# Optimization experiments

Measured on AMD Instinct MI355X. Metric: run time of the kernel, lower is better.

## Reference

```python
import jax, jax.numpy as jnp
import numpy as np

N, E, D, DH, MH, MO = 100000, 1600000, 128, 512, 512, 128
EPS_BN = 1e-5
EPS_LN = 1e-5


def setup_inputs() -> dict:
    key = jax.random.key(0)
    ks = jax.random.split(key, 16)
    def lin(k, fan_in, shape):
        return jax.random.normal(k, shape, jnp.float32) / np.sqrt(fan_in)
    return {
        'x': jax.random.normal(ks[0], (N, D), jnp.float32),
        'src': jax.random.randint(ks[1], (E,), 0, N, jnp.int32),
        'dst': jax.random.randint(ks[2], (E,), 0, N, jnp.int32),
        'gcn_w': lin(ks[3], D, (D, D)),
        'gcn_b': jnp.zeros((D,), jnp.float32),
        'ff_w1': lin(ks[4], D, (D, DH)),
        'ff_b1': jnp.zeros((DH,), jnp.float32),
        'ln_g': jnp.ones((DH,), jnp.float32),
        'ln_b': jnp.zeros((DH,), jnp.float32),
        'ff_w2': lin(ks[5], DH, (DH, D)),
        'ff_b2': jnp.zeros((D,), jnp.float32),
        'fc1_w': lin(ks[6], D, (D, MH)),
        'fc1_b': jnp.zeros((MH,), jnp.float32),
        'bn1_g': jnp.ones((MH,), jnp.float32),
        'bn1_b': jnp.zeros((MH,), jnp.float32),
        'fc2_w': lin(ks[7], MH, (MH, MH)),
        'fc2_b': jnp.zeros((MH,), jnp.float32),
        'bn2_g': jnp.ones((MH,), jnp.float32),
        'bn2_b': jnp.zeros((MH,), jnp.float32),
        'fc3_w': lin(ks[8], MH, (MH, MO)),
        'fc3_b': jnp.zeros((MO,), jnp.float32),
        'bn3_g': jnp.ones((MO,), jnp.float32),
        'bn3_b': jnp.zeros((MO,), jnp.float32),
        'fc4_w': lin(ks[9], MO, (MO, 1)),
        'fc4_b': jnp.zeros((1,), jnp.float32),
    }


def _gelu(x):
    return jax.nn.gelu(x, approximate=False)  # torch nn.GELU default (erf)


def _batchnorm(x, g, b):
    # BatchNorm1d in training mode: batch statistics, biased variance
    m = jnp.mean(x, axis=0)
    v = jnp.var(x, axis=0)
    return (x - m) * jax.lax.rsqrt(v + EPS_BN) * g + b


def reference(x, src, dst, gcn_w, gcn_b, ff_w1, ff_b1, ln_g, ln_b, ff_w2, ff_b2,
              fc1_w, fc1_b, bn1_g, bn1_b, fc2_w, fc2_b, bn2_g, bn2_b,
              fc3_w, fc3_b, bn3_g, bn3_b, fc4_w, fc4_b):
    n = x.shape[0]
    ones = jnp.ones(src.shape[0], x.dtype)
    out_deg = jnp.clip(jax.ops.segment_sum(ones, src, num_segments=n), 1.0)
    in_deg = jnp.clip(jax.ops.segment_sum(ones, dst, num_segments=n), 1.0)
    # GraphConv, norm='both': left-normalize, aggregate, matmul (in==out), right-normalize, bias
    h = x * (out_deg ** -0.5)[:, None]
    agg = jax.ops.segment_sum(h[src], dst, num_segments=n)  # [N, D]
    h = agg @ gcn_w
    h = h * (in_deg ** -0.5)[:, None] + gcn_b
    # FeedForwardLayer: lin1 -> GELU -> LayerNorm -> lin2
    f = _gelu(h @ ff_w1 + ff_b1)
    mu = jnp.mean(f, axis=-1, keepdims=True)
    var = jnp.var(f, axis=-1, keepdims=True)
    f = (f - mu) * jax.lax.rsqrt(var + EPS_LN) * ln_g + ln_b
    h = f @ ff_w2 + ff_b2  # [N, D]
    # MLP head
    h = _batchnorm(_gelu(h @ fc1_w + fc1_b), bn1_g, bn1_b)
    h = _batchnorm(_gelu(h @ fc2_w + fc2_b), bn2_g, bn2_b)
    h = _batchnorm(_gelu(h @ fc3_w + fc3_b), bn3_g, bn3_b)
    return h @ fc4_w + fc4_b  # [N, 1]
```

## Files before the change

kernel.cpp:

```cpp
#include <hip/hip_runtime.h>
#include <hip/hip_bf16.h>

#define N_NODES 100000
#define NPAD    100096
#define NRB     782
#define E_EDGES 1600000
#define NBLK_SCAN 98

#define HNR  4
#define HP   64
#define HCHK 25000
#define HRSZ 32768

#define AS1 __attribute__((address_space(1)))
#define AS3 __attribute__((address_space(3)))

typedef unsigned int   uint;
typedef unsigned short ushort;
typedef __attribute__((ext_vector_type(8))) short bfx8;
typedef __attribute__((ext_vector_type(4))) float fx4;

__device__ __forceinline__ float bf2f(ushort u) {
    return __uint_as_float(((uint)u) << 16);
}
__device__ __forceinline__ ushort f2bf(float f) {
    uint x = __float_as_uint(f);
    return (ushort)((x + 0x7FFFu + ((x >> 16) & 1u)) >> 16);
}
__device__ __forceinline__ float gelu_fast(float x) {
    float u = 1.5957691f * __builtin_fmaf(0.044715f * x * x, x, x);
    return x / (1.0f + __expf(-u));
}
__device__ __forceinline__ float wave_sum(float v) {
    #pragma unroll
    for (int m = 1; m < 64; m <<= 1) v += __shfl_xor(v, m, 64);
    return v;
}
__device__ __forceinline__ int xcd_swz(int orig, int nwg) {
    int q = nwg >> 3, r = nwg & 7;
    int x = orig & 7, o = orig >> 3;
    return (x < r ? x * (q + 1) : r * (q + 1) + (x - r) * q) + o;
}

__global__ void k_hist(const int* __restrict__ idx, uint* __restrict__ part)
{
    __shared__ uint h[HRSZ / 2];
    int c = blockIdx.x & (HP - 1);
    int r = blockIdx.x / HP;
    int t = threadIdx.x;
    for (int i = t; i < HRSZ / 2; i += 256) h[i] = 0u;
    __syncthreads();
    int base = r << 15;
    int e0 = c * HCHK;
    for (int e = e0 + t; e < e0 + HCHK; e += 256) {
        int v = idx[e] - base;
        if ((uint)v < (uint)HRSZ)
            atomicAdd(&h[v >> 1], 1u << ((v & 1) * 16));
    }
    __syncthreads();
    uint* dst = part + ((size_t)blockIdx.x << 14);
    for (int i = t; i < HRSZ / 2; i += 256) dst[i] = h[i];
}

__global__ void k_degmerge(const uint* __restrict__ partO, const uint* __restrict__ partI,
                           int* __restrict__ inc, float* __restrict__ oscale,
                           float* __restrict__ ininv)
{
    int n = blockIdx.x * 256 + threadIdx.x;
    if (n >= NPAD) return;
    int r = n >> 15, i = (n & 32767) >> 1, hi = (n & 1) * 16;
    const uint* po = partO + ((size_t)(r * HP) << 14) + i;
    const uint* pi = partI + ((size_t)(r * HP) << 14) + i;
    uint so = 0, si = 0;
    for (int c = 0; c < HP; ++c) {
        so += (po[(size_t)c << 14] >> hi) & 0xffffu;
        si += (pi[(size_t)c << 14] >> hi) & 0xffffu;
    }
    inc[n] = (int)si;
    oscale[n] = rsqrtf((float)max((int)so, 1));
    ininv[n] = rsqrtf((float)max((int)si, 1));
}

__global__ void k_scan1(const int* __restrict__ inc, int* __restrict__ coff, int* __restrict__ btot)
{
    __shared__ int a[1024], bsh[1024];
    int t = threadIdx.x;
    int i = blockIdx.x * 1024 + t;
    a[t] = (i < N_NODES) ? inc[i] : 0;
    __syncthreads();
    int* s = a; int* d = bsh;
    for (int dd = 1; dd < 1024; dd <<= 1) {
        int v = s[t] + ((t >= dd) ? s[t - dd] : 0);
        d[t] = v;
        __syncthreads();
        int* tmp = s; s = d; d = tmp;
    }
    if (i < N_NODES) coff[i + 1] = s[t];
    if (t == 1023) btot[blockIdx.x] = s[t];
}

__global__ void k_scan2(int* __restrict__ btot)
{
    __shared__ int a[128], bsh[128];
    int t = threadIdx.x;
    a[t] = (t < NBLK_SCAN) ? btot[t] : 0;
    __syncthreads();
    int* s = a; int* d = bsh;
    for (int dd = 1; dd < 128; dd <<= 1) {
        int v = s[t] + ((t >= dd) ? s[t - dd] : 0);
        d[t] = v;
        __syncthreads();
        int* tmp = s; s = d; d = tmp;
    }
    if (t < NBLK_SCAN) btot[t] = s[t];
}

__global__ void k_scan3(int* __restrict__ coff, const int* __restrict__ btot)
{
    int i = blockIdx.x * 256 + threadIdx.x;
    if (i == 0) coff[0] = 0;
    if (i < N_NODES) {
        int blk = i >> 10;
        if (blk > 0) coff[i + 1] += btot[blk - 1];
    }
}

__global__ void k_fill(const int* __restrict__ src, const int* __restrict__ dst,
                       const int* __restrict__ coff, int* __restrict__ cur, int* __restrict__ eidx)
{
    int e = blockIdx.x * 256 + threadIdx.x;
    if (e < E_EDGES) {
        int d = dst[e];
        int p = coff[d] + atomicAdd(&cur[d], 1);
        eidx[p] = src[e];
    }
}

__global__ void k_xhat(const float* __restrict__ x, const float* __restrict__ oscale,
                       ushort* __restrict__ xh)
{
    size_t i = (size_t)blockIdx.x * 256 + threadIdx.x;
    size_t e0 = i * 4;
    int row = (int)(e0 >> 7);
    uint2 o;
    if (row < N_NODES) {
        float4 v = *(const float4*)(x + e0);
        float s = oscale[row];
        o.x = (uint)f2bf(v.x * s) | ((uint)f2bf(v.y * s) << 16);
        o.y = (uint)f2bf(v.z * s) | ((uint)f2bf(v.w * s) << 16);
    } else {
        o.x = 0u; o.y = 0u;
    }
    *(uint2*)(xh + e0) = o;
}

__global__ void k_agg(const int* __restrict__ off, const int* __restrict__ eidx,
                      const ushort* __restrict__ xh, ushort* __restrict__ agg)
{
    int wid = threadIdx.x >> 6, lane = threadIdx.x & 63;
    int r = blockIdx.x * 4 + wid;
    if (r >= NPAD) return;
    int f = lane & 15;
    int g = lane >> 4;
    float a[8] = {0.f, 0.f, 0.f, 0.f, 0.f, 0.f, 0.f, 0.f};
    if (r < N_NODES) {
        int s = off[r], e = off[r + 1];
        for (int i = s + g; i < e; i += 4) {
            int sv = eidx[i];
            bfx8 v = *(const bfx8*)(xh + (size_t)sv * 128 + f * 8);
            #pragma unroll
            for (int k = 0; k < 8; ++k) a[k] += bf2f((ushort)v[k]);
        }
    }
    #pragma unroll
    for (int k = 0; k < 8; ++k) {
        a[k] += __shfl_xor(a[k], 16, 64);
        a[k] += __shfl_xor(a[k], 32, 64);
    }
    if (g == 0) {
        bfx8 o;
        #pragma unroll
        for (int k = 0; k < 8; ++k) o[k] = (short)f2bf(a[k]);
        *(bfx8*)(agg + (size_t)r * 128 + f * 8) = o;
    }
}

__global__ void k_wT(const float* __restrict__ W, int K, int M, ushort* __restrict__ Wt)
{
    int id = blockIdx.x * 256 + threadIdx.x;
    if (id < K * M) {
        int m = id / K, k = id - m * K;
        Wt[id] = f2bf(W[(size_t)k * M + m]);
    }
}

__global__ void k_wT_ln(const float* __restrict__ W, const float* __restrict__ g,
                        const float* __restrict__ b, const float* __restrict__ b2,
                        ushort* __restrict__ Wt, float* __restrict__ u, float* __restrict__ t)
{
    int wid = threadIdx.x >> 6, lane = threadIdx.x & 63;
    int m = blockIdx.x * 4 + wid;
    if (m >= 128) return;
    float us = 0.f, ts = 0.f;
    for (int k = lane; k < 512; k += 64) {
        float w = W[(size_t)k * 128 + m];
        float gk = g[k], bk = b[k];
        Wt[(size_t)m * 512 + k] = f2bf(gk * w);
        us += gk * w; ts += bk * w;
    }
    us = wave_sum(us); ts = wave_sum(ts);
    if (lane == 0) { u[m] = us; t[m] = ts + b2[m]; }
}

template <int K1, int EPI1, int STATS2>
__global__ __launch_bounds__(256, 2) void k_fused(
    const ushort* __restrict__ A1, const ushort* __restrict__ B1t,
    const ushort* __restrict__ B2t, ushort* __restrict__ C,
    const float* __restrict__ c1v0, const float* __restrict__ r1v0,
    const float* __restrict__ r1v1, const float* __restrict__ c1v1,
    const float* __restrict__ bias2,
    float* __restrict__ lnS, float* __restrict__ lnC,
    float* __restrict__ pS, float* __restrict__ pQ)
{
    __shared__ __align__(16) char smem[32768 + 32768 + 2048];
    char* A2 = smem;
    char* S  = smem + 32768;
    float* st_s = (float*)(smem + 65536);
    float* st_q = (float*)(smem + 65536 + 1024);

    const int rb = xcd_swz(blockIdx.x, gridDim.x);
    const int tid = threadIdx.x;
    const int lane = tid & 63;
    const int wid = tid >> 6;
    const int m0 = (wid >> 1) * 64;
    const int n0 = (wid & 1) * 64;
    const int frl = lane & 15;
    const int kg = lane >> 4;

    char* As = S;
    char* Bs = S + 16384;
    fx4 acc[4][4] = {};
    const ushort* Arow0 = A1 + (size_t)(rb * 128) * K1;

    for (int kb = 0; kb < K1; kb += 64) {
        #pragma unroll
        for (int c = 0; c < 4; ++c) {
            int b = c * 4096 + tid * 16;
            int row = b >> 7;
            int cibs = (b & 127) ^ ((row & 7) << 4);
            const char* ga = (const char*)(Arow0 + (size_t)row * K1 + kb) + cibs;
            const char* gb = (const char*)(B1t + (size_t)row * K1 + kb) + cibs;
            char* la = As + c * 4096 + (wid << 10);
            char* lb = Bs + c * 4096 + (wid << 10);
            __builtin_amdgcn_global_load_lds((const AS1 void*)ga, (AS3 void*)la, 16, 0, 0);
            __builtin_amdgcn_global_load_lds((const AS1 void*)gb, (AS3 void*)lb, 16, 0, 0);
        }
        __syncthreads();
        #pragma unroll
        for (int kk = 0; kk < 2; ++kk) {
            bfx8 av[4], bv[4];
            #pragma unroll
            for (int i = 0; i < 4; ++i) {
                int ar = m0 + i * 16 + frl;
                int ab = (ar * 128 + kk * 64 + kg * 16) ^ ((ar & 7) << 4);
                av[i] = *(const bfx8*)(As + ab);
                int br = n0 + i * 16 + frl;
                int bb = (br * 128 + kk * 64 + kg * 16) ^ ((br & 7) << 4);
                bv[i] = *(const bfx8*)(Bs + bb);
            }
            #pragma unroll
            for (int i = 0; i < 4; ++i)
                #pragma unroll
                for (int j = 0; j < 4; ++j)
                    acc[i][j] = __builtin_amdgcn_mfma_f32_16x16x32_bf16(av[i], bv[j], acc[i][j], 0, 0, 0);
        }
        __syncthreads();
    }

    #pragma unroll
    for (int j = 0; j < 4; ++j) {
        int colL = n0 + j * 16 + frl;
        float c0 = c1v0[colL];
        float c1 = (EPI1 == 3) ? c1v1[colL] : 0.f;
        #pragma unroll
        for (int i = 0; i < 4; ++i) {
            int rbaseL = m0 + i * 16 + kg * 4;
            #pragma unroll
            for (int r = 0; r < 4; ++r) {
                float v = acc[i][j][r];
                int rowL = rbaseL + r;
                int grow = rb * 128 + rowL;
                if (EPI1 == 0) v = v * r1v0[grow] + c0;
                else           v = r1v0[grow] * v + r1v1[grow] * c1 + c0;
                *(ushort*)(A2 + rowL * 256 + ((colL * 2) ^ ((rowL & 7) << 4))) = f2bf(v);
            }
        }
    }
    __syncthreads();

    float rs = 0.f, rq = 0.f;
    const int rowR = tid >> 1, halfR = tid & 1;

    for (int cb2 = 0; cb2 < 4; ++cb2) {
        #pragma unroll
        for (int c = 0; c < 8; ++c) {
            int b = c * 4096 + tid * 16;
            int row = b >> 8;
            int cibs = (b & 255) ^ ((row & 7) << 4);
            const char* gb = (const char*)(B2t + (size_t)(cb2 * 128 + row) * 128) + cibs;
            char* lb = S + c * 4096 + (wid << 10);
            __builtin_amdgcn_global_load_lds((const AS1 void*)gb, (AS3 void*)lb, 16, 0, 0);
        }
        __syncthreads();

        fx4 a2[4][4] = {};
        #pragma unroll
        for (int kk = 0; kk < 4; ++kk) {
            bfx8 av[4], bv[4];
            int c2 = kk * 64 + kg * 16;
            #pragma unroll
            for (int i = 0; i < 4; ++i) {
                int ar = m0 + i * 16 + frl;
                av[i] = *(const bfx8*)(A2 + ar * 256 + (c2 ^ ((ar & 7) << 4)));
                int br = n0 + i * 16 + frl;
                bv[i] = *(const bfx8*)(S + br * 256 + (c2 ^ ((br & 7) << 4)));
            }
            #pragma unroll
            for (int i = 0; i < 4; ++i)
                #pragma unroll
                for (int j = 0; j < 4; ++j)
                    a2[i][j] = __builtin_amdgcn_mfma_f32_16x16x32_bf16(av[i], bv[j], a2[i][j], 0, 0, 0);
        }
        __syncthreads();

        float sL[4] = {0.f, 0.f, 0.f, 0.f}, qL[4] = {0.f, 0.f, 0.f, 0.f};
        #pragma unroll
        for (int j = 0; j < 4; ++j) {
            int colL = n0 + j * 16 + frl;
            float bcol = bias2[cb2 * 128 + colL];
            #pragma unroll
            for (int i = 0; i < 4; ++i) {
                int rbaseL = m0 + i * 16 + kg * 4;
                #pragma unroll
                for (int r = 0; r < 4; ++r) {
                    float v = gelu_fast(a2[i][j][r] + bcol);
                    int rowL = rbaseL + r;
                    if (STATS2 == 1) {
                        if (rb * 128 + rowL < N_NODES) { sL[j] += v; qL[j] += v * v; }
                    }
                    *(ushort*)(S + rowL * 256 + ((colL * 2) ^ ((rowL & 7) << 4))) = f2bf(v);
                }
            }
            if (STATS2 == 1) {
                float s = sL[j], q = qL[j];
                s += __shfl_xor(s, 16, 64); s += __shfl_xor(s, 32, 64);
                q += __shfl_xor(q, 16, 64); q += __shfl_xor(q, 32, 64);
                if (kg == 0) {
                    st_s[(wid >> 1) * 128 + n0 + j * 16 + frl] = s;
                    st_q[(wid >> 1) * 128 + n0 + j * 16 + frl] = q;
                }
            }
        }
        __syncthreads();

        {
            int r2 = tid >> 4;
            int s2 = tid & 15;
            #pragma unroll
            for (int pass = 0; pass < 8; ++pass) {
                int rowL = pass * 16 + r2;
                int boff = rowL * 256 + ((s2 * 16) ^ ((rowL & 7) << 4));
                bfx8 v = *(const bfx8*)(S + boff);
                *(bfx8*)((char*)(C + (size_t)(rb * 128 + rowL) * 512 + cb2 * 128) + s2 * 16) = v;
            }
        }
        if (STATS2 == 1 && tid < 128) {
            size_t pidx = ((size_t)rb * 4 + cb2) * 128 + tid;
            pS[pidx] = st_s[tid] + st_s[128 + tid];
            pQ[pidx] = st_q[tid] + st_q[128 + tid];
        }
        if (STATS2 == 2) {
            #pragma unroll
            for (int ss = 0; ss < 8; ++ss) {
                int boff = rowR * 256 + (((halfR * 64 + ss * 8) * 2) ^ ((rowR & 7) << 4));
                bfx8 v = *(const bfx8*)(S + boff);
                #pragma unroll
                for (int k2 = 0; k2 < 8; ++k2) {
                    float f = bf2f((ushort)v[k2]);
                    rs += f; rq += f * f;
                }
            }
        }
        __syncthreads();
    }

    if (STATS2 == 2) {
        rs += __shfl_xor(rs, 1, 64);
        rq += __shfl_xor(rq, 1, 64);
        if (halfR == 0) {
            float mean = rs * (1.f / 512.f);
            float var = fmaxf(rq * (1.f / 512.f) - mean * mean, 0.f);
            float sr = rsqrtf(var + 1e-5f);
            int grow = rb * 128 + rowR;
            lnS[grow] = sr;
            lnC[grow] = -mean * sr;
        }
    }
}

template <int EPI, int STATS>
__global__ __launch_bounds__(256, 4) void k_gemm(
    const ushort* __restrict__ A, const ushort* __restrict__ Bt,
    ushort* __restrict__ C, int K, int M,
    const float* __restrict__ colv0, const float* __restrict__ rowv0,
    float* __restrict__ pS, float* __restrict__ pQ, int grb0)
{
    __shared__ __align__(16) char smem[32768 + (STATS == 1 ? 1024 : 0)];
    char* AsB = smem;
    char* BsB = smem + 16384;

    const int nwg = gridDim.x;
    const int wgid = xcd_swz(blockIdx.x, nwg);
    const int nCB = M >> 7;
    const int cb = wgid % nCB;
    const int rb = wgid / nCB;
    const int tid = threadIdx.x;
    const int lane = tid & 63;
    const int wid = tid >> 6;
    const int m0 = (wid >> 1) * 64;
    const int n0 = (wid & 1) * 64;
    const int frl = lane & 15;
    const int kg = lane >> 4;

    float* statsf = (float*)(smem + 32768);
    if (STATS == 1 && tid < 128) { statsf[tid] = 0.f; statsf[128 + tid] = 0.f; }

    fx4 acc[4][4] = {};

    const ushort* Arow0 = A + (size_t)(rb * 128) * K;
    const ushort* Brow0 = Bt + (size_t)(cb * 128) * K;

    for (int kb = 0; kb < K; kb += 64) {
        #pragma unroll
        for (int c = 0; c < 4; ++c) {
            int b = c * 4096 + tid * 16;
            int row = b >> 7;
            int cibs = (b & 127) ^ ((row & 7) << 4);
            const char* ga = (const char*)(Arow0 + (size_t)row * K + kb) + cibs;
            const char* gb = (const char*)(Brow0 + (size_t)row * K + kb) + cibs;
            char* la = AsB + c * 4096 + (wid << 10);
            char* lb = BsB + c * 4096 + (wid << 10);
            __builtin_amdgcn_global_load_lds((const AS1 void*)ga, (AS3 void*)la, 16, 0, 0);
            __builtin_amdgcn_global_load_lds((const AS1 void*)gb, (AS3 void*)lb, 16, 0, 0);
        }
        __syncthreads();
        #pragma unroll
        for (int kk = 0; kk < 2; ++kk) {
            bfx8 av[4], bv[4];
            #pragma unroll
            for (int i = 0; i < 4; ++i) {
                int ar = m0 + i * 16 + frl;
                int ab = (ar * 128 + kk * 64 + kg * 16) ^ ((ar & 7) << 4);
                av[i] = *(const bfx8*)(AsB + ab);
                int br = n0 + i * 16 + frl;
                int bb = (br * 128 + kk * 64 + kg * 16) ^ ((br & 7) << 4);
                bv[i] = *(const bfx8*)(BsB + bb);
            }
            #pragma unroll
            for (int i = 0; i < 4; ++i)
                #pragma unroll
                for (int j = 0; j < 4; ++j)
                    acc[i][j] = __builtin_amdgcn_mfma_f32_16x16x32_bf16(av[i], bv[j], acc[i][j], 0, 0, 0);
        }
        __syncthreads();
    }

    float sL[4] = {0.f, 0.f, 0.f, 0.f}, qL[4] = {0.f, 0.f, 0.f, 0.f};
    #pragma unroll
    for (int j = 0; j < 4; ++j) {
        int colL = n0 + j * 16 + frl;
        float c0 = colv0[cb * 128 + colL];
        #pragma unroll
        for (int i = 0; i < 4; ++i) {
            int rbaseL = m0 + i * 16 + kg * 4;
            #pragma unroll
            for (int r = 0; r < 4; ++r) {
                float v = acc[i][j][r];
                int rowL = rbaseL + r;
                int grow = (grb0 + rb) * 128 + rowL;
                if (EPI == 0) v = v * rowv0[grow] + c0;
                else          v = gelu_fast(v + c0);
                if (STATS == 1) {
                    if (grow < N_NODES) { sL[j] += v; qL[j] += v * v; }
                }
                int boff = rowL * 256 + ((colL * 2) ^ ((rowL & 7) << 4));
                *(ushort*)(smem + boff) = f2bf(v);
            }
        }
    }
    if (STATS == 1) {
        #pragma unroll
        for (int j = 0; j < 4; ++j) {
            float s = sL[j], q = qL[j];
            s += __shfl_xor(s, 16, 64); s += __shfl_xor(s, 32, 64);
            q += __shfl_xor(q, 16, 64); q += __shfl_xor(q, 32, 64);
            if (kg == 0) {
                atomicAdd(&statsf[n0 + j * 16 + frl], s);
                atomicAdd(&statsf[128 + n0 + j * 16 + frl], q);
            }
        }
    }
    __syncthreads();
    {
        int r2 = tid >> 4;
        int s2 = tid & 15;
        #pragma unroll
        for (int pass = 0; pass < 8; ++pass) {
            int rowL = pass * 16 + r2;
            int boff = rowL * 256 + ((s2 * 16) ^ ((rowL & 7) << 4));
            bfx8 v = *(const bfx8*)(smem + boff);
            *(bfx8*)((char*)(C + (size_t)(rb * 128 + rowL) * M + cb * 128) + s2 * 16) = v;
        }
    }
    if (STATS == 1 && tid < 128) {
        size_t pidx = ((size_t)(grb0 + rb) * nCB + cb) * 128 + tid;
        pS[pidx] = statsf[tid];
        pQ[pidx] = statsf[128 + tid];
    }
}

__global__ void k_colmerge(const float* __restrict__ pS, const float* __restrict__ pQ,
                           float* __restrict__ oS, float* __restrict__ oQ, int M)
{
    int wid = threadIdx.x >> 6, lane = threadIdx.x & 63;
    int m = blockIdx.x * 4 + wid;
    if (m >= M) return;
    int nCB = M >> 7, cb = m >> 7, colL = m & 127;
    float s = 0.f, q = 0.f;
    for (int rb = lane; rb < NRB; rb += 64) {
        size_t idx = ((size_t)rb * nCB + cb) * 128 + colL;
        s += pS[idx]; q += pQ[idx];
    }
    s = wave_sum(s); q = wave_sum(q);
    if (lane == 0) { oS[m] = s; oQ[m] = q; }
}

__global__ void k_fold(const float* __restrict__ W, const float* __restrict__ bw,
                       const float* __restrict__ g, const float* __restrict__ bb,
                       const float* __restrict__ sum, const float* __restrict__ sqs,
                       int K, int M, ushort* __restrict__ WtO, float* __restrict__ bO)
{
    int wid = threadIdx.x >> 6, lane = threadIdx.x & 63;
    int m = blockIdx.x * 4 + wid;
    if (m >= M) return;
    float acc = 0.f;
    for (int k = lane; k < K; k += 64) {
        float mean = sum[k] * (1.f / (float)N_NODES);
        float var = sqs[k] * (1.f / (float)N_NODES) - mean * mean;
        float s = g[k] * rsqrtf(var + 1e-5f);
        float t = bb[k] - mean * s;
        float w = W[(size_t)k * M + m];
        WtO[(size_t)m * K + k] = f2bf(w * s);
        acc += t * w;
    }
    acc = wave_sum(acc);
    if (lane == 0) bO[m] = bw[m] + acc;
}

__global__ void k_out(const ushort* __restrict__ m3, const ushort* __restrict__ w4,
                      const float* __restrict__ b4, float* __restrict__ out)
{
    int wid = threadIdx.x >> 6, lane = threadIdx.x & 63;
    int r = blockIdx.x * 4 + wid;
    if (r >= N_NODES) return;
    uint u = *(const uint*)(m3 + (size_t)r * 128 + lane * 2);
    uint w = *(const uint*)(w4 + lane * 2);
    float acc = bf2f((ushort)(u & 0xffffu)) * bf2f((ushort)(w & 0xffffu))
              + bf2f((ushort)(u >> 16)) * bf2f((ushort)(w >> 16));
    acc = wave_sum(acc);
    if (lane == 0) out[r] = acc + b4[0];
}

extern "C" void kernel_launch(void* const* d_in, const int* in_sizes, int n_in,
                              void* d_out, int out_size, void* d_ws, size_t ws_size,
                              hipStream_t stream)
{
    const float* x     = (const float*)d_in[0];
    const int*   src   = (const int*)d_in[1];
    const int*   dst   = (const int*)d_in[2];
    const float* gcn_w = (const float*)d_in[3];
    const float* gcn_b = (const float*)d_in[4];
    const float* ff_w1 = (const float*)d_in[5];
    const float* ff_b1 = (const float*)d_in[6];
    const float* ln_g  = (const float*)d_in[7];
    const float* ln_b  = (const float*)d_in[8];
    const float* ff_w2 = (const float*)d_in[9];
    const float* ff_b2 = (const float*)d_in[10];
    const float* fc1_w = (const float*)d_in[11];
    const float* fc1_b = (const float*)d_in[12];
    const float* bn1_g = (const float*)d_in[13];
    const float* bn1_b = (const float*)d_in[14];
    const float* fc2_w = (const float*)d_in[15];
    const float* fc2_b = (const float*)d_in[16];
    const float* bn2_g = (const float*)d_in[17];
    const float* bn2_b = (const float*)d_in[18];
    const float* fc3_w = (const float*)d_in[19];
    const float* fc3_b = (const float*)d_in[20];
    const float* bn3_g = (const float*)d_in[21];
    const float* bn3_b = (const float*)d_in[22];
    const float* fc4_w = (const float*)d_in[23];
    const float* fc4_b = (const float*)d_in[24];
    float* out = (float*)d_out;
    (void)in_sizes; (void)n_in; (void)out_size;

    char* base = (char*)d_ws;
    char* p = base;
    auto alloc = [&](size_t bytes) -> char* {
        char* r = p;
        p += (bytes + 255) & ~(size_t)255;
        return r;
    };
    int*    inc    = (int*)alloc((size_t)NPAD * 4);
    int*    cur    = (int*)alloc((size_t)NPAD * 4);
    int*    coff   = (int*)alloc(((size_t)NPAD + 1) * 4);
    int*    btot   = (int*)alloc(128 * 4);
    int*    eidx   = (int*)alloc((size_t)E_EDGES * 4);
    float*  oscale = (float*)alloc((size_t)NPAD * 4);
    float*  ininv  = (float*)alloc((size_t)NPAD * 4);
    float*  bns    = (float*)alloc(6 * 512 * 4);
    float*  b2p    = (float*)alloc(512 * 4);
    float*  b3p    = (float*)alloc(128 * 4);
    float*  b4p    = (float*)alloc(4);
    float*  lnS    = (float*)alloc((size_t)NPAD * 4);
    float*  lnC    = (float*)alloc((size_t)NPAD * 4);
    float*  lnU    = (float*)alloc(128 * 4);
    float*  lnT    = (float*)alloc(128 * 4);
    float*  pS     = (float*)alloc((size_t)4 * NPAD * 4);
    float*  pQ     = (float*)alloc((size_t)4 * NPAD * 4);
    ushort* gwT    = (ushort*)alloc(128 * 128 * 2);
    ushort* ff1T   = (ushort*)alloc(512 * 128 * 2);
    ushort* ff2T   = (ushort*)alloc(128 * 512 * 2);
    ushort* fc1T   = (ushort*)alloc(512 * 128 * 2);
    ushort* fc2T   = (ushort*)alloc(512 * 512 * 2);
    ushort* fc3T   = (ushort*)alloc(128 * 512 * 2);
    ushort* w4t    = (ushort*)alloc(128 * 2);
    ushort* buf1   = (ushort*)alloc((size_t)NPAD * 128 * 2);
    ushort* bufC   = (ushort*)alloc((size_t)NPAD * 512 * 2);

    size_t used = (size_t)(p - base);
    bool   sep  = (used + (size_t)NPAD * 512 * 2) <= ws_size;
    ushort* m2  = sep ? (ushort*)alloc((size_t)NPAD * 512 * 2) : bufC;

    uint* partO = (uint*)bufC;
    uint* partI = partO + (size_t)HNR * HP * (HRSZ / 2);
    ushort* xh  = bufC;
    ushort* agg = buf1;

    float* bn1s = bns;
    float* bn1q = bns + 512;
    float* bn2s = bns + 1024;
    float* bn2q = bns + 1536;
    float* bn3s = bns + 2048;
    float* bn3q = bns + 2560;

    hipMemsetAsync(cur, 0, (size_t)NPAD * 4, stream);

    k_hist<<<HNR * HP, 256, 0, stream>>>(src, partO);
    k_hist<<<HNR * HP, 256, 0, stream>>>(dst, partI);
    k_degmerge<<<(NPAD + 255) / 256, 256, 0, stream>>>(partO, partI, inc, oscale, ininv);
    k_scan1<<<NBLK_SCAN, 1024, 0, stream>>>(inc, coff, btot);
    k_scan2<<<1, 128, 0, stream>>>(btot);
    k_scan3<<<(N_NODES + 255) / 256, 256, 0, stream>>>(coff, btot);
    k_fill<<<E_EDGES / 256, 256, 0, stream>>>(src, dst, coff, cur, eidx);
    k_xhat<<<(NPAD / 256) * 32, 256, 0, stream>>>(x, oscale, xh);
    k_agg<<<NPAD / 4, 256, 0, stream>>>(coff, eidx, xh, agg);

    k_wT<<<(128 * 128) / 256, 256, 0, stream>>>(gcn_w, 128, 128, gwT);
    k_wT<<<(128 * 512) / 256, 256, 0, stream>>>(ff_w1, 128, 512, ff1T);
    k_wT<<<(128 * 512) / 256, 256, 0, stream>>>(fc1_w, 128, 512, fc1T);
    k_wT_ln<<<32, 256, 0, stream>>>(ff_w2, ln_g, ln_b, ff_b2, ff2T, lnU, lnT);

    k_fused<128, 0, 2><<<NRB, 256, 0, stream>>>(agg, gwT, ff1T, bufC,
                                                gcn_b, ininv, nullptr, nullptr, ff_b1,
                                                lnS, lnC, nullptr, nullptr);
    k_fused<512, 3, 1><<<NRB, 256, 0, stream>>>(bufC, ff2T, fc1T, bufC,
                                                lnT, lnS, lnC, lnU, fc1_b,
                                                nullptr, nullptr, pS, pQ);
    k_colmerge<<<128, 256, 0, stream>>>(pS, pQ, bn1s, bn1q, 512);
    k_fold<<<512 / 4, 256, 0, stream>>>(fc2_w, fc2_b, bn1_g, bn1_b, bn1s, bn1q, 512, 512, fc2T, b2p);
    if (sep) {
        k_gemm<1, 1><<<4 * NRB, 256, 0, stream>>>(bufC, fc2T, m2, 512, 512,
                                                  b2p, nullptr, pS, pQ, 0);
    } else {
        const int cOff[6] = {0, 195, 390, 585, 780, 782};
        for (int c = 0; c < 5; ++c) {
            int rb0 = cOff[c], nrb = cOff[c + 1] - rb0;
            k_gemm<1, 1><<<nrb * 4, 256, 0, stream>>>(bufC + (size_t)rb0 * 128 * 512, fc2T,
                                                      buf1, 512, 512,
                                                      b2p, nullptr, pS, pQ, rb0);
            hipMemcpyAsync(bufC + (size_t)rb0 * 128 * 512, buf1,
                           (size_t)nrb * 128 * 512 * 2, hipMemcpyDeviceToDevice, stream);
        }
    }
    k_colmerge<<<128, 256, 0, stream>>>(pS, pQ, bn2s, bn2q, 512);
    k_fold<<<128 / 4, 256, 0, stream>>>(fc3_w, fc3_b, bn2_g, bn2_b, bn2s, bn2q, 512, 128, fc3T, b3p);
    k_gemm<1, 1><<<NRB, 256, 0, stream>>>(m2, fc3T, buf1, 512, 128,
                                          b3p, nullptr, pS, pQ, 0);
    k_colmerge<<<32, 256, 0, stream>>>(pS, pQ, bn3s, bn3q, 128);
    k_fold<<<1, 256, 0, stream>>>(fc4_w, fc4_b, bn3_g, bn3_b, bn3s, bn3q, 128, 1, w4t, b4p);
    k_out<<<N_NODES / 4, 256, 0, stream>>>(buf1, w4t, b4p, out);
}
```

Baseline: 679.1 us.

## Replace global-atomic CSR fill with two-pass bucketed partition and local-atomic scatter

```diff
diff --git a/kernel.cpp b/kernel.cpp
--- a/kernel.cpp
+++ b/kernel.cpp
@@ -11,6 +11,9 @@
 #define HP   64
 #define HCHK 25000
 #define HRSZ 32768
+
+#define NBK  196
+#define PCHK 6250
 
 #define AS1 __attribute__((address_space(1)))
 #define AS3 __attribute__((address_space(3)))
@@ -125,14 +128,73 @@
     }
 }
 
-__global__ void k_fill(const int* __restrict__ src, const int* __restrict__ dst,
-                       const int* __restrict__ coff, int* __restrict__ cur, int* __restrict__ eidx)
-{
-    int e = blockIdx.x * 256 + threadIdx.x;
-    if (e < E_EDGES) {
-        int d = dst[e];
-        int p = coff[d] + atomicAdd(&cur[d], 1);
-        eidx[p] = src[e];
+__global__ void k_curinit(const int* __restrict__ coff, int* __restrict__ gcur)
+{
+    int t = threadIdx.x;
+    if (t < NBK) gcur[t] = coff[t << 9];
+}
+
+__global__ __launch_bounds__(256) void k_part(const int* __restrict__ src, const int* __restrict__ dst,
+                                              int* __restrict__ gcur, uint* __restrict__ tmp)
+{
+    __shared__ int cnt[NBK], rcnt[NBK], base[NBK], loff[NBK];
+    __shared__ int sa[256], sb[256];
+    __shared__ uint arr[PCHK];
+    int t = threadIdx.x;
+    if (t < NBK) { cnt[t] = 0; rcnt[t] = 0; }
+    __syncthreads();
+    int e0 = blockIdx.x * PCHK;
+    for (int e = e0 + t; e < e0 + PCHK; e += 256)
+        atomicAdd(&cnt[dst[e] >> 9], 1);
+    __syncthreads();
+    sa[t] = (t < NBK) ? cnt[t] : 0;
+    __syncthreads();
+    int* s = sa; int* d = sb;
+    for (int dd = 1; dd < 256; dd <<= 1) {
+        int v = s[t] + ((t >= dd) ? s[t - dd] : 0);
+        d[t] = v;
+        __syncthreads();
+        int* w = s; s = d; d = w;
+    }
+    if (t < NBK) {
+        loff[t] = s[t] - cnt[t];
+        base[t] = atomicAdd(&gcur[t], cnt[t]);
+    }
+    __syncthreads();
+    for (int e = e0 + t; e < e0 + PCHK; e += 256) {
+        int dv = dst[e];
+        int b = dv >> 9;
+        int r = atomicAdd(&rcnt[b], 1);
+        arr[loff[b] + r] = ((uint)src[e] << 9) | (uint)(dv & 511);
+    }
+    __syncthreads();
+    for (int b = 0; b < NBK; ++b) {
+        int n = cnt[b], lo = loff[b], gb = base[b];
+        for (int i = t; i < n; i += 256)
+            tmp[gb + i] = arr[lo + i];
+    }
+}
+
+__global__ __launch_bounds__(256) void k_fill2(const uint* __restrict__ tmp, const int* __restrict__ coff,
+                                               int* __restrict__ eidx)
+{
+    __shared__ int lco[512];
+    __shared__ int lcnt[512];
+    int b = blockIdx.x, t = threadIdx.x;
+    int n0 = b << 9;
+    for (int i = t; i < 512; i += 256) {
+        int node = n0 + i;
+        lco[i] = (node <= N_NODES) ? coff[node] : E_EDGES;
+        lcnt[i] = 0;
+    }
+    __syncthreads();
+    int s0 = coff[n0];
+    int s1 = (n0 + 512 <= N_NODES) ? coff[n0 + 512] : E_EDGES;
+    for (int e = s0 + t; e < s1; e += 256) {
+        uint v = tmp[e];
+        int dl = v & 511;
+        int r = atomicAdd(&lcnt[dl], 1);
+        eidx[lco[dl] + r] = (int)(v >> 9);
     }
 }
 
@@ -621,9 +683,9 @@
         return r;
     };
     int*    inc    = (int*)alloc((size_t)NPAD * 4);
-    int*    cur    = (int*)alloc((size_t)NPAD * 4);
     int*    coff   = (int*)alloc(((size_t)NPAD + 1) * 4);
     int*    btot   = (int*)alloc(128 * 4);
+    int*    gcur   = (int*)alloc(256 * 4);
     int*    eidx   = (int*)alloc((size_t)E_EDGES * 4);
     float*  oscale = (float*)alloc((size_t)NPAD * 4);
     float*  ininv  = (float*)alloc((size_t)NPAD * 4);
@@ -653,6 +715,7 @@
 
     uint* partO = (uint*)bufC;
     uint* partI = partO + (size_t)HNR * HP * (HRSZ / 2);
+    uint* etmp  = (uint*)bufC;
     ushort* xh  = bufC;
     ushort* agg = buf1;
 
@@ -663,15 +726,15 @@
     float* bn3s = bns + 2048;
     float* bn3q = bns + 2560;
 
-    hipMemsetAsync(cur, 0, (size_t)NPAD * 4, stream);
-
     k_hist<<<HNR * HP, 256, 0, stream>>>(src, partO);
     k_hist<<<HNR * HP, 256, 0, stream>>>(dst, partI);
     k_degmerge<<<(NPAD + 255) / 256, 256, 0, stream>>>(partO, partI, inc, oscale, ininv);
     k_scan1<<<NBLK_SCAN, 1024, 0, stream>>>(inc, coff, btot);
     k_scan2<<<1, 128, 0, stream>>>(btot);
     k_scan3<<<(N_NODES + 255) / 256, 256, 0, stream>>>(coff, btot);
-    k_fill<<<E_EDGES / 256, 256, 0, stream>>>(src, dst, coff, cur, eidx);
+    k_curinit<<<1, 256, 0, stream>>>(coff, gcur);
+    k_part<<<E_EDGES / PCHK, 256, 0, stream>>>(src, dst, gcur, etmp);
+    k_fill2<<<NBK, 256, 0, stream>>>(etmp, coff, eidx);
     k_xhat<<<(NPAD / 256) * 32, 256, 0, stream>>>(x, oscale, xh);
     k_agg<<<NPAD / 4, 256, 0, stream>>>(coff, eidx, xh, agg);
 
```

Measured after the change: 672.8 us. No clear change (-0.9%).
